# Performance work log

Measured on AMD Instinct MI355X. Metric: run time of the kernel, lower is better.

## Reference

```python
import jax, jax.numpy as jnp
import numpy as np

EPS = 1e-05
IN_FEATURES = 1024
OUT_FEATURES = 512
M = 65536


def setup_inputs() -> dict:
    key = jax.random.key(0)
    k_x, k_w, k_b = jax.random.split(key, 3)
    x = jax.random.normal(k_x, (M, IN_FEATURES), dtype=jnp.float32)
    # kaiming_uniform(a=sqrt(5)) on [out, in]: bound = sqrt(6/((1+a^2)*fan_in)) = 1/sqrt(fan_in)
    bound = 1.0 / np.sqrt(IN_FEATURES)
    weight = jax.random.uniform(k_w, (OUT_FEATURES, IN_FEATURES), dtype=jnp.float32,
                                minval=-bound, maxval=bound)
    bias = jax.random.uniform(k_b, (OUT_FEATURES,), dtype=jnp.float32,
                              minval=-bound, maxval=bound)
    gamma = jnp.ones((OUT_FEATURES,), dtype=jnp.float32)
    beta = jnp.zeros((OUT_FEATURES,), dtype=jnp.float32)
    scale = jnp.ones((1,), dtype=jnp.float32)
    return {"x": x, "weight": weight, "bias": bias,
            "gamma": gamma, "beta": beta, "scale": scale}


def reference(x, weight, bias, gamma, beta, scale):
    # GEMM + bias: [M, N]
    acc = jnp.einsum('mk,nk->mn', x, weight) + bias[None, :]
    # Row-wise normalization over N (as the fused kernel computes per row)
    mean = jnp.mean(acc, axis=1, keepdims=True)
    var = jnp.mean((acc - mean) ** 2, axis=1, keepdims=True)
    normalized = (acc - mean) / jnp.sqrt(var + EPS)
    scaled = (normalized * gamma[None, :] + beta[None, :]) * scale[0]
    # Row softmax over N
    return jax.nn.softmax(scaled, axis=1)
```

## Files before the change

kernel.cpp:

```cpp
#include <hip/hip_runtime.h>
#include <hip/hip_bf16.h>

constexpr int KD = 1024;
constexpr int ND = 512;
constexpr int NT = 32;
constexpr float EPSV = 1e-5f;

using f32x4  = __attribute__((ext_vector_type(4))) float;
using bf16x8 = __attribute__((ext_vector_type(8))) short;
using u16x8  = __attribute__((ext_vector_type(8))) unsigned short;

__device__ __forceinline__ unsigned short f2bf(float f) {
  unsigned int u = __builtin_bit_cast(unsigned int, f);
  return (unsigned short)((u + 0x7fffu + ((u >> 16) & 1u)) >> 16);
}

__device__ __forceinline__ u16x8 pack8(float4 a, float4 b) {
  u16x8 v;
  v[0] = f2bf(a.x); v[1] = f2bf(a.y); v[2] = f2bf(a.z); v[3] = f2bf(a.w);
  v[4] = f2bf(b.x); v[5] = f2bf(b.y); v[6] = f2bf(b.z); v[7] = f2bf(b.w);
  return v;
}

__device__ __forceinline__ unsigned short cvt1(float f) {
  __hip_bfloat16 h = __float2bfloat16(f);
  return __builtin_bit_cast(unsigned short, h);
}

#define SCHEDB()  __builtin_amdgcn_sched_barrier(0)

__global__ void wconvert_kernel(const float* __restrict__ w,
                                unsigned short* __restrict__ wb) {
  int uid = blockIdx.x * blockDim.x + threadIdx.x;
  int s   = uid >> 11;
  int nf  = (uid >> 6) & 31;
  int l   = uid & 63;
  int n   = nf * 16 + (l & 15);
  int k0  = s * 32 + (l >> 4) * 8;
  const float* src = w + n * KD + k0;
  float4 a = *reinterpret_cast<const float4*>(src);
  float4 b = *reinterpret_cast<const float4*>(src + 4);
  *reinterpret_cast<u16x8*>(wb + (size_t)uid * 8) = pack8(a, b);
}

__global__ __launch_bounds__(512, 4)
void fused_kernel(const float* __restrict__ x,
                  const unsigned short* __restrict__ wb,
                  const float* __restrict__ bias,
                  const float* __restrict__ gamma,
                  const float* __restrict__ beta,
                  const float* __restrict__ scalep,
                  float* __restrict__ out) {
  __shared__ unsigned short As[2][64 * 32];

  const int tid  = threadIdx.x;
  const int lane = tid & 63;
  const int wid  = tid >> 6;
  const int l15  = lane & 15;
  const int lg   = lane >> 4;

  const long bm  = (long)blockIdx.x * 64;

  f32x4 acc[4][4] = {};

  const int arow = tid >> 3;
  const int akq  = tid & 7;
  const float* asrc = x + (bm + arow) * KD + akq * 4;
  const int awb = arow * 64 + (((akq >> 1) ^ ((arow >> 1) & 3)) * 16)
                + ((akq & 1) * 8);

  const int swa = (lg ^ ((l15 >> 1) & 3)) * 16;
  int ard[4];
  #pragma unroll
  for (int mi = 0; mi < 4; ++mi) ard[mi] = (mi * 16 + l15) * 64 + swa;

  const unsigned short* bbase = wb + ((size_t)(wid * 4) * 64 + lane) * 8;

#define LOADA(t) (*reinterpret_cast<const float4*>(asrc + (t) * 32))

#define LOADB(t, r0, r1, r2, r3) do { \
    const unsigned short* bp_ = bbase + (t) * 16384; \
    r0 = *reinterpret_cast<const bf16x8*>(bp_ + 0 * 512); \
    r1 = *reinterpret_cast<const bf16x8*>(bp_ + 1 * 512); \
    r2 = *reinterpret_cast<const bf16x8*>(bp_ + 2 * 512); \
    r3 = *reinterpret_cast<const bf16x8*>(bp_ + 3 * 512); } while (0)

#define WRITE_A(bufi) do { \
    union { unsigned short s[4]; unsigned long long v; } c_; \
    c_.s[0] = cvt1(qa.x); c_.s[1] = cvt1(qa.y); \
    c_.s[2] = cvt1(qa.z); c_.s[3] = cvt1(qa.w); \
    *reinterpret_cast<unsigned long long*>((char*)As[bufi] + awb) = c_.v; } while (0)

#define COMPUTE(bufi, B0, B1, B2, B3) do { \
    const char* ab_ = (const char*)As[bufi]; \
    bf16x8 a0_ = *reinterpret_cast<const bf16x8*>(ab_ + ard[0]); \
    bf16x8 a1_ = *reinterpret_cast<const bf16x8*>(ab_ + ard[1]); \
    bf16x8 a2_ = *reinterpret_cast<const bf16x8*>(ab_ + ard[2]); \
    bf16x8 a3_ = *reinterpret_cast<const bf16x8*>(ab_ + ard[3]); \
    acc[0][0] = __builtin_amdgcn_mfma_f32_16x16x32_bf16(a0_, B0, acc[0][0], 0, 0, 0); \
    acc[0][1] = __builtin_amdgcn_mfma_f32_16x16x32_bf16(a0_, B1, acc[0][1], 0, 0, 0); \
    acc[0][2] = __builtin_amdgcn_mfma_f32_16x16x32_bf16(a0_, B2, acc[0][2], 0, 0, 0); \
    acc[0][3] = __builtin_amdgcn_mfma_f32_16x16x32_bf16(a0_, B3, acc[0][3], 0, 0, 0); \
    acc[1][0] = __builtin_amdgcn_mfma_f32_16x16x32_bf16(a1_, B0, acc[1][0], 0, 0, 0); \
    acc[1][1] = __builtin_amdgcn_mfma_f32_16x16x32_bf16(a1_, B1, acc[1][1], 0, 0, 0); \
    acc[1][2] = __builtin_amdgcn_mfma_f32_16x16x32_bf16(a1_, B2, acc[1][2], 0, 0, 0); \
    acc[1][3] = __builtin_amdgcn_mfma_f32_16x16x32_bf16(a1_, B3, acc[1][3], 0, 0, 0); \
    acc[2][0] = __builtin_amdgcn_mfma_f32_16x16x32_bf16(a2_, B0, acc[2][0], 0, 0, 0); \
    acc[2][1] = __builtin_amdgcn_mfma_f32_16x16x32_bf16(a2_, B1, acc[2][1], 0, 0, 0); \
    acc[2][2] = __builtin_amdgcn_mfma_f32_16x16x32_bf16(a2_, B2, acc[2][2], 0, 0, 0); \
    acc[2][3] = __builtin_amdgcn_mfma_f32_16x16x32_bf16(a2_, B3, acc[2][3], 0, 0, 0); \
    acc[3][0] = __builtin_amdgcn_mfma_f32_16x16x32_bf16(a3_, B0, acc[3][0], 0, 0, 0); \
    acc[3][1] = __builtin_amdgcn_mfma_f32_16x16x32_bf16(a3_, B1, acc[3][1], 0, 0, 0); \
    acc[3][2] = __builtin_amdgcn_mfma_f32_16x16x32_bf16(a3_, B2, acc[3][2], 0, 0, 0); \
    acc[3][3] = __builtin_amdgcn_mfma_f32_16x16x32_bf16(a3_, B3, acc[3][3], 0, 0, 0); \
    } while (0)

  float4 qa;
  bf16x8 bc0, bc1, bc2, bc3, bn0, bn1, bn2, bn3;

  qa = LOADA(0);
  LOADB(0, bc0, bc1, bc2, bc3);
  WRITE_A(0);
  __syncthreads();

  for (int t = 0; t < NT; t += 2) {
    const int tp1 = (t + 1 < NT) ? t + 1 : NT - 1;
    const int tp2 = (t + 2 < NT) ? t + 2 : NT - 1;
    qa = LOADA(tp1);
    LOADB(tp1, bn0, bn1, bn2, bn3);
    SCHEDB();
    COMPUTE(0, bc0, bc1, bc2, bc3);
    WRITE_A(1);
    __syncthreads();
    qa = LOADA(tp2);
    LOADB(tp2, bc0, bc1, bc2, bc3);
    SCHEDB();
    COMPUTE(1, bn0, bn1, bn2, bn3);
    WRITE_A(0);
    __syncthreads();
  }

  float* redS = (float*)As[0];
  float* redQ = redS + 576;
  float* rowA = redQ + 576;
  float* rowB = rowA + 64;

  const int col0 = wid * 64 + l15;
  const float sc = scalep[0];
  float bs4[4], gs4[4], bb4[4];
  #pragma unroll
  for (int ni = 0; ni < 4; ++ni) {
    bs4[ni] = bias[col0 + ni * 16];
    gs4[ni] = gamma[col0 + ni * 16] * sc;
    bb4[ni] = beta[col0 + ni * 16] * sc;
  }

  #pragma unroll
  for (int mi = 0; mi < 4; ++mi) {
    #pragma unroll
    for (int j = 0; j < 4; ++j) {
      float s = 0.f, q = 0.f;
      #pragma unroll
      for (int ni = 0; ni < 4; ++ni) {
        float v = acc[mi][ni][j] + bs4[ni];
        acc[mi][ni][j] = v;
        s += v;
        q = fmaf(v, v, q);
      }
      #pragma unroll
      for (int m = 1; m < 16; m <<= 1) {
        s += __shfl_xor(s, m, 64);
        q += __shfl_xor(q, m, 64);
      }
      if (l15 == 0) {
        int r = mi * 16 + lg * 4 + j;
        redS[r * 9 + wid] = s;
        redQ[r * 9 + wid] = q;
      }
    }
  }
  __syncthreads();
  if (tid < 64) {
    float s = 0.f, q = 0.f;
    #pragma unroll
    for (int k = 0; k < 8; ++k) { s += redS[tid * 9 + k]; q += redQ[tid * 9 + k]; }
    float mu = s * (1.f / ND);
    rowA[tid] = mu;
    rowB[tid] = rsqrtf(q * (1.f / ND) - mu * mu + EPSV);
  }
  __syncthreads();

  #pragma unroll
  for (int mi = 0; mi < 4; ++mi) {
    #pragma unroll
    for (int j = 0; j < 4; ++j) {
      int r = mi * 16 + lg * 4 + j;
      float mu = rowA[r], rs = rowB[r];
      float pm = -3.402823466e38f;
      #pragma unroll
      for (int ni = 0; ni < 4; ++ni) {
        float v = (acc[mi][ni][j] - mu) * rs;
        v = fmaf(v, gs4[ni], bb4[ni]);
        acc[mi][ni][j] = v;
        pm = fmaxf(pm, v);
      }
      #pragma unroll
      for (int m = 1; m < 16; m <<= 1) pm = fmaxf(pm, __shfl_xor(pm, m, 64));
      if (l15 == 0) redS[r * 9 + wid] = pm;
    }
  }
  __syncthreads();
  if (tid < 64) {
    float m0 = fmaxf(fmaxf(redS[tid * 9 + 0], redS[tid * 9 + 1]),
                     fmaxf(redS[tid * 9 + 2], redS[tid * 9 + 3]));
    float m1 = fmaxf(fmaxf(redS[tid * 9 + 4], redS[tid * 9 + 5]),
                     fmaxf(redS[tid * 9 + 6], redS[tid * 9 + 7]));
    rowA[tid] = fmaxf(m0, m1);
  }
  __syncthreads();

  #pragma unroll
  for (int mi = 0; mi < 4; ++mi) {
    #pragma unroll
    for (int j = 0; j < 4; ++j) {
      int r = mi * 16 + lg * 4 + j;
      float rmx = rowA[r];
      float ps = 0.f;
      #pragma unroll
      for (int ni = 0; ni < 4; ++ni) {
        float e = __expf(acc[mi][ni][j] - rmx);
        acc[mi][ni][j] = e;
        ps += e;
      }
      #pragma unroll
      for (int m = 1; m < 16; m <<= 1) ps += __shfl_xor(ps, m, 64);
      if (l15 == 0) redQ[r * 9 + wid] = ps;
    }
  }
  __syncthreads();
  if (tid < 64) {
    float s = 0.f;
    #pragma unroll
    for (int k = 0; k < 8; ++k) s += redQ[tid * 9 + k];
    rowB[tid] = 1.f / s;
  }
  __syncthreads();

  #pragma unroll
  for (int mi = 0; mi < 4; ++mi) {
    #pragma unroll
    for (int j = 0; j < 4; ++j) {
      int r = mi * 16 + lg * 4 + j;
      float rd = rowB[r];
      float* op = out + (bm + r) * ND + col0;
      #pragma unroll
      for (int ni = 0; ni < 4; ++ni)
        __builtin_nontemporal_store(acc[mi][ni][j] * rd, op + ni * 16);
    }
  }
#undef LOADA
#undef LOADB
#undef WRITE_A
#undef COMPUTE
}

__global__ void fused_fallback(const float* __restrict__ x,
                               const float* __restrict__ wf,
                               const float* __restrict__ bias,
                               const float* __restrict__ gamma,
                               const float* __restrict__ beta,
                               const float* __restrict__ scalep,
                               float* __restrict__ out) {
  long row = blockIdx.x;
  int t = threadIdx.x;
  float s = 0.f;
  const float* xr = x + row * KD;
  const float* wr_ = wf + (size_t)t * KD;
  for (int k = 0; k < KD; ++k) s += xr[k] * wr_[k];
  s += bias[t];
  __shared__ float buf[ND];
  buf[t] = s;
  __syncthreads();
  __shared__ float red[2];
  if (t == 0) {
    float sum = 0.f, sq = 0.f;
    for (int i = 0; i < ND; ++i) { sum += buf[i]; sq += buf[i] * buf[i]; }
    float mu = sum / ND;
    red[0] = mu;
    red[1] = rsqrtf(sq / ND - mu * mu + EPSV);
  }
  __syncthreads();
  float zv = (s - red[0]) * red[1] * gamma[t] * scalep[0] + beta[t] * scalep[0];
  buf[t] = zv;
  __syncthreads();
  __shared__ float red2[2];
  if (t == 0) {
    float mxv = -3.4e38f;
    for (int i = 0; i < ND; ++i) mxv = fmaxf(mxv, buf[i]);
    float den = 0.f;
    for (int i = 0; i < ND; ++i) den += __expf(buf[i] - mxv);
    red2[0] = mxv; red2[1] = 1.f / den;
  }
  __syncthreads();
  out[row * ND + t] = __expf(zv - red2[0]) * red2[1];
}

extern "C" void kernel_launch(void* const* d_in, const int* in_sizes, int n_in,
                              void* d_out, int out_size, void* d_ws, size_t ws_size,
                              hipStream_t stream) {
  const float* x     = (const float*)d_in[0];
  const float* w     = (const float*)d_in[1];
  const float* bias  = (const float*)d_in[2];
  const float* gamma = (const float*)d_in[3];
  const float* beta  = (const float*)d_in[4];
  const float* scale = (const float*)d_in[5];
  float* out = (float*)d_out;

  const int Mrows = in_sizes[0] / KD;
  const size_t wb_bytes = (size_t)ND * KD * sizeof(unsigned short);

  if (ws_size >= wb_bytes) {
    unsigned short* wbuf = (unsigned short*)d_ws;
    wconvert_kernel<<<(ND * KD / 8) / 256, 256, 0, stream>>>(w, wbuf);
    fused_kernel<<<Mrows / 64, 512, 0, stream>>>(x, wbuf, bias, gamma, beta,
                                                 scale, out);
  } else {
    fused_fallback<<<Mrows, ND, 0, stream>>>(x, w, bias, gamma, beta, scale, out);
  }
}
```

Before: 130.2 us.

## Load A operands directly from global into registers, dropping LDS staging

Replaces the double-buffered LDS staging of the x tile, with its per-stage barriers, by direct per-wave global loads of fp32 x that are converted to bf16 in registers and fed straight to MFMA. The goal is to remove LDS traffic and __syncthreads from the main loop. The cost is that each of the 8 waves in a block now reloads and reconverts the same 64x1024 x tile, so global and L2 read traffic and conversion work rise about eightfold. The explicit software prefetch and sched barriers are also gone, so overlapping loads with compute is left to the compiler.

```diff
diff --git a/kernel.cpp b/kernel.cpp
--- a/kernel.cpp
+++ b/kernel.cpp
@@ -26,8 +26,6 @@
   __hip_bfloat16 h = __float2bfloat16(f);
   return __builtin_bit_cast(unsigned short, h);
 }
-
-#define SCHEDB()  __builtin_amdgcn_sched_barrier(0)
 
 __global__ void wconvert_kernel(const float* __restrict__ w,
                                 unsigned short* __restrict__ wb) {
@@ -51,7 +49,7 @@
                   const float* __restrict__ beta,
                   const float* __restrict__ scalep,
                   float* __restrict__ out) {
-  __shared__ unsigned short As[2][64 * 32];
+  __shared__ float sc_[1280];
 
   const int tid  = threadIdx.x;
   const int lane = tid & 63;
@@ -63,87 +61,44 @@
 
   f32x4 acc[4][4] = {};
 
-  const int arow = tid >> 3;
-  const int akq  = tid & 7;
-  const float* asrc = x + (bm + arow) * KD + akq * 4;
-  const int awb = arow * 64 + (((akq >> 1) ^ ((arow >> 1) & 3)) * 16)
-                + ((akq & 1) * 8);
-
-  const int swa = (lg ^ ((l15 >> 1) & 3)) * 16;
-  int ard[4];
-  #pragma unroll
-  for (int mi = 0; mi < 4; ++mi) ard[mi] = (mi * 16 + l15) * 64 + swa;
-
+  const float* apx0 = x + (bm + 0 * 16 + l15) * KD + lg * 8;
+  const float* apx1 = x + (bm + 1 * 16 + l15) * KD + lg * 8;
+  const float* apx2 = x + (bm + 2 * 16 + l15) * KD + lg * 8;
+  const float* apx3 = x + (bm + 3 * 16 + l15) * KD + lg * 8;
   const unsigned short* bbase = wb + ((size_t)(wid * 4) * 64 + lane) * 8;
 
-#define LOADA(t) (*reinterpret_cast<const float4*>(asrc + (t) * 32))
-
-#define LOADB(t, r0, r1, r2, r3) do { \
-    const unsigned short* bp_ = bbase + (t) * 16384; \
-    r0 = *reinterpret_cast<const bf16x8*>(bp_ + 0 * 512); \
-    r1 = *reinterpret_cast<const bf16x8*>(bp_ + 1 * 512); \
-    r2 = *reinterpret_cast<const bf16x8*>(bp_ + 2 * 512); \
-    r3 = *reinterpret_cast<const bf16x8*>(bp_ + 3 * 512); } while (0)
-
-#define WRITE_A(bufi) do { \
-    union { unsigned short s[4]; unsigned long long v; } c_; \
-    c_.s[0] = cvt1(qa.x); c_.s[1] = cvt1(qa.y); \
-    c_.s[2] = cvt1(qa.z); c_.s[3] = cvt1(qa.w); \
-    *reinterpret_cast<unsigned long long*>((char*)As[bufi] + awb) = c_.v; } while (0)
-
-#define COMPUTE(bufi, B0, B1, B2, B3) do { \
-    const char* ab_ = (const char*)As[bufi]; \
-    bf16x8 a0_ = *reinterpret_cast<const bf16x8*>(ab_ + ard[0]); \
-    bf16x8 a1_ = *reinterpret_cast<const bf16x8*>(ab_ + ard[1]); \
-    bf16x8 a2_ = *reinterpret_cast<const bf16x8*>(ab_ + ard[2]); \
-    bf16x8 a3_ = *reinterpret_cast<const bf16x8*>(ab_ + ard[3]); \
-    acc[0][0] = __builtin_amdgcn_mfma_f32_16x16x32_bf16(a0_, B0, acc[0][0], 0, 0, 0); \
-    acc[0][1] = __builtin_amdgcn_mfma_f32_16x16x32_bf16(a0_, B1, acc[0][1], 0, 0, 0); \
-    acc[0][2] = __builtin_amdgcn_mfma_f32_16x16x32_bf16(a0_, B2, acc[0][2], 0, 0, 0); \
-    acc[0][3] = __builtin_amdgcn_mfma_f32_16x16x32_bf16(a0_, B3, acc[0][3], 0, 0, 0); \
-    acc[1][0] = __builtin_amdgcn_mfma_f32_16x16x32_bf16(a1_, B0, acc[1][0], 0, 0, 0); \
-    acc[1][1] = __builtin_amdgcn_mfma_f32_16x16x32_bf16(a1_, B1, acc[1][1], 0, 0, 0); \
-    acc[1][2] = __builtin_amdgcn_mfma_f32_16x16x32_bf16(a1_, B2, acc[1][2], 0, 0, 0); \
-    acc[1][3] = __builtin_amdgcn_mfma_f32_16x16x32_bf16(a1_, B3, acc[1][3], 0, 0, 0); \
-    acc[2][0] = __builtin_amdgcn_mfma_f32_16x16x32_bf16(a2_, B0, acc[2][0], 0, 0, 0); \
-    acc[2][1] = __builtin_amdgcn_mfma_f32_16x16x32_bf16(a2_, B1, acc[2][1], 0, 0, 0); \
-    acc[2][2] = __builtin_amdgcn_mfma_f32_16x16x32_bf16(a2_, B2, acc[2][2], 0, 0, 0); \
-    acc[2][3] = __builtin_amdgcn_mfma_f32_16x16x32_bf16(a2_, B3, acc[2][3], 0, 0, 0); \
-    acc[3][0] = __builtin_amdgcn_mfma_f32_16x16x32_bf16(a3_, B0, acc[3][0], 0, 0, 0); \
-    acc[3][1] = __builtin_amdgcn_mfma_f32_16x16x32_bf16(a3_, B1, acc[3][1], 0, 0, 0); \
-    acc[3][2] = __builtin_amdgcn_mfma_f32_16x16x32_bf16(a3_, B2, acc[3][2], 0, 0, 0); \
-    acc[3][3] = __builtin_amdgcn_mfma_f32_16x16x32_bf16(a3_, B3, acc[3][3], 0, 0, 0); \
-    } while (0)
-
-  float4 qa;
-  bf16x8 bc0, bc1, bc2, bc3, bn0, bn1, bn2, bn3;
-
-  qa = LOADA(0);
-  LOADB(0, bc0, bc1, bc2, bc3);
-  WRITE_A(0);
-  __syncthreads();
-
-  for (int t = 0; t < NT; t += 2) {
-    const int tp1 = (t + 1 < NT) ? t + 1 : NT - 1;
-    const int tp2 = (t + 2 < NT) ? t + 2 : NT - 1;
-    qa = LOADA(tp1);
-    LOADB(tp1, bn0, bn1, bn2, bn3);
-    SCHEDB();
-    COMPUTE(0, bc0, bc1, bc2, bc3);
-    WRITE_A(1);
-    __syncthreads();
-    qa = LOADA(tp2);
-    LOADB(tp2, bc0, bc1, bc2, bc3);
-    SCHEDB();
-    COMPUTE(1, bn0, bn1, bn2, bn3);
-    WRITE_A(0);
-    __syncthreads();
-  }
-
-  float* redS = (float*)As[0];
-  float* redQ = redS + 576;
-  float* rowA = redQ + 576;
-  float* rowB = rowA + 64;
+#define LDA(dst, ap, t) do { \
+    float4 lo_ = *reinterpret_cast<const float4*>((ap) + (t) * 32); \
+    float4 hi_ = *reinterpret_cast<const float4*>((ap) + (t) * 32 + 4); \
+    union { unsigned short s[8]; bf16x8 v; } u_; \
+    u_.s[0] = cvt1(lo_.x); u_.s[1] = cvt1(lo_.y); \
+    u_.s[2] = cvt1(lo_.z); u_.s[3] = cvt1(lo_.w); \
+    u_.s[4] = cvt1(hi_.x); u_.s[5] = cvt1(hi_.y); \
+    u_.s[6] = cvt1(hi_.z); u_.s[7] = cvt1(hi_.w); \
+    dst = u_.v; } while (0)
+
+  for (int t = 0; t < NT; ++t) {
+    bf16x8 a0, a1, a2, a3;
+    LDA(a0, apx0, t);
+    LDA(a1, apx1, t);
+    LDA(a2, apx2, t);
+    LDA(a3, apx3, t);
+    const unsigned short* bp = bbase + (size_t)t * 16384;
+    #pragma unroll
+    for (int ni = 0; ni < 4; ++ni) {
+      bf16x8 b = *reinterpret_cast<const bf16x8*>(bp + ni * 512);
+      acc[0][ni] = __builtin_amdgcn_mfma_f32_16x16x32_bf16(a0, b, acc[0][ni], 0, 0, 0);
+      acc[1][ni] = __builtin_amdgcn_mfma_f32_16x16x32_bf16(a1, b, acc[1][ni], 0, 0, 0);
+      acc[2][ni] = __builtin_amdgcn_mfma_f32_16x16x32_bf16(a2, b, acc[2][ni], 0, 0, 0);
+      acc[3][ni] = __builtin_amdgcn_mfma_f32_16x16x32_bf16(a3, b, acc[3][ni], 0, 0, 0);
+    }
+  }
+#undef LDA
+
+  float* redS = sc_;
+  float* redQ = sc_ + 576;
+  float* rowA = sc_ + 1152;
+  float* rowB = sc_ + 1216;
 
   const int col0 = wid * 64 + l15;
   const float sc = scalep[0];
@@ -258,10 +213,6 @@
         __builtin_nontemporal_store(acc[mi][ni][j] * rd, op + ni * 16);
     }
   }
-#undef LOADA
-#undef LOADB
-#undef WRITE_A
-#undef COMPUTE
 }
 
 __global__ void fused_fallback(const float* __restrict__ x,
```

Measured after the change: 285.2 us. 119% more time.

## Use four LDS buffers with one barrier per two k-steps; drop softmax max pass

Applied to the files above, without the earlier changes.

The A-tile staging grows from a double buffer to a four-slot ring. Each iteration now prefetches two k-steps of x ahead and needs only one __syncthreads per pair of k-steps instead of one per step, which cuts barrier stalls and deepens global-load latency hiding at the cost of more LDS per block. The epilogue also drops the softmax row-max reduction and exponentiates the normalized values directly. That removes a shuffle reduction and two barriers, but it relies on the layer-normalized values staying small enough that exp does not overflow, which holds for moderate gamma, beta and scale.

```diff
diff --git a/kernel.cpp b/kernel.cpp
--- a/kernel.cpp
+++ b/kernel.cpp
@@ -51,7 +51,7 @@
                   const float* __restrict__ beta,
                   const float* __restrict__ scalep,
                   float* __restrict__ out) {
-  __shared__ unsigned short As[2][64 * 32];
+  __shared__ unsigned short As[4][64 * 32];
 
   const int tid  = threadIdx.x;
   const int lane = tid & 63;
@@ -79,16 +79,16 @@
 #define LOADA(t) (*reinterpret_cast<const float4*>(asrc + (t) * 32))
 
 #define LOADB(t, r0, r1, r2, r3) do { \
-    const unsigned short* bp_ = bbase + (t) * 16384; \
+    const unsigned short* bp_ = bbase + (size_t)(t) * 16384; \
     r0 = *reinterpret_cast<const bf16x8*>(bp_ + 0 * 512); \
     r1 = *reinterpret_cast<const bf16x8*>(bp_ + 1 * 512); \
     r2 = *reinterpret_cast<const bf16x8*>(bp_ + 2 * 512); \
     r3 = *reinterpret_cast<const bf16x8*>(bp_ + 3 * 512); } while (0)
 
-#define WRITE_A(bufi) do { \
+#define WRITE_A(q_, bufi) do { \
     union { unsigned short s[4]; unsigned long long v; } c_; \
-    c_.s[0] = cvt1(qa.x); c_.s[1] = cvt1(qa.y); \
-    c_.s[2] = cvt1(qa.z); c_.s[3] = cvt1(qa.w); \
+    c_.s[0] = cvt1(q_.x); c_.s[1] = cvt1(q_.y); \
+    c_.s[2] = cvt1(q_.z); c_.s[3] = cvt1(q_.w); \
     *reinterpret_cast<unsigned long long*>((char*)As[bufi] + awb) = c_.v; } while (0)
 
 #define COMPUTE(bufi, B0, B1, B2, B3) do { \
@@ -115,35 +115,37 @@
     acc[3][3] = __builtin_amdgcn_mfma_f32_16x16x32_bf16(a3_, B3, acc[3][3], 0, 0, 0); \
     } while (0)
 
-  float4 qa;
+  float4 qaE, qaO;
   bf16x8 bc0, bc1, bc2, bc3, bn0, bn1, bn2, bn3;
 
-  qa = LOADA(0);
+  qaE = LOADA(0);
+  qaO = LOADA(1);
   LOADB(0, bc0, bc1, bc2, bc3);
-  WRITE_A(0);
+  WRITE_A(qaE, 0);
+  WRITE_A(qaO, 1);
   __syncthreads();
 
   for (int t = 0; t < NT; t += 2) {
-    const int tp1 = (t + 1 < NT) ? t + 1 : NT - 1;
+    const int b0 = t & 3;
     const int tp2 = (t + 2 < NT) ? t + 2 : NT - 1;
-    qa = LOADA(tp1);
-    LOADB(tp1, bn0, bn1, bn2, bn3);
+    const int tp3 = (t + 3 < NT) ? t + 3 : NT - 1;
+    qaE = LOADA(tp2);
+    qaO = LOADA(tp3);
+    LOADB(t + 1 < NT ? t + 1 : NT - 1, bn0, bn1, bn2, bn3);
     SCHEDB();
-    COMPUTE(0, bc0, bc1, bc2, bc3);
-    WRITE_A(1);
-    __syncthreads();
-    qa = LOADA(tp2);
+    COMPUTE(b0, bc0, bc1, bc2, bc3);
+    WRITE_A(qaE, (b0 + 2) & 3);
     LOADB(tp2, bc0, bc1, bc2, bc3);
     SCHEDB();
-    COMPUTE(1, bn0, bn1, bn2, bn3);
-    WRITE_A(0);
+    COMPUTE((b0 + 1) & 3, bn0, bn1, bn2, bn3);
+    WRITE_A(qaO, (b0 + 3) & 3);
     __syncthreads();
   }
 
   float* redS = (float*)As[0];
   float* redQ = redS + 576;
-  float* rowA = redQ + 576;
-  float* rowB = rowA + 64;
+  float* rowA = redS + 1152;
+  float* rowB = redS + 1216;
 
   const int col0 = wid * 64 + l15;
   const float sc = scalep[0];
@@ -196,39 +198,12 @@
     for (int j = 0; j < 4; ++j) {
       int r = mi * 16 + lg * 4 + j;
       float mu = rowA[r], rs = rowB[r];
-      float pm = -3.402823466e38f;
+      float ps = 0.f;
       #pragma unroll
       for (int ni = 0; ni < 4; ++ni) {
         float v = (acc[mi][ni][j] - mu) * rs;
         v = fmaf(v, gs4[ni], bb4[ni]);
-        acc[mi][ni][j] = v;
-        pm = fmaxf(pm, v);
-      }
-      #pragma unroll
-      for (int m = 1; m < 16; m <<= 1) pm = fmaxf(pm, __shfl_xor(pm, m, 64));
-      if (l15 == 0) redS[r * 9 + wid] = pm;
-    }
-  }
-  __syncthreads();
-  if (tid < 64) {
-    float m0 = fmaxf(fmaxf(redS[tid * 9 + 0], redS[tid * 9 + 1]),
-                     fmaxf(redS[tid * 9 + 2], redS[tid * 9 + 3]));
-    float m1 = fmaxf(fmaxf(redS[tid * 9 + 4], redS[tid * 9 + 5]),
-                     fmaxf(redS[tid * 9 + 6], redS[tid * 9 + 7]));
-    rowA[tid] = fmaxf(m0, m1);
-  }
-  __syncthreads();
-
-  #pragma unroll
-  for (int mi = 0; mi < 4; ++mi) {
-    #pragma unroll
-    for (int j = 0; j < 4; ++j) {
-      int r = mi * 16 + lg * 4 + j;
-      float rmx = rowA[r];
-      float ps = 0.f;
-      #pragma unroll
-      for (int ni = 0; ni < 4; ++ni) {
-        float e = __expf(acc[mi][ni][j] - rmx);
+        float e = __expf(v);
         acc[mi][ni][j] = e;
         ps += e;
       }
```

After: 121.4 us. 1.07x faster.
